# Performance work log

Hardware: AMD Instinct MI355X
Metric: run time of the kernel (lower is better)

The kernel has to match this reference:

```python
import jax, jax.numpy as jnp
import numpy as np

N, E, B = 16000, 256000, 32
IN, HID, H1, OUT, H2 = 768, 256, 4, 128, 2
LN_EPS = 1e-5


def _gat_layer(x, src, dst, W, a_src, a_dst, b, heads, out, n, concat):
    # x: (n, in), W: (heads*out, in), a_src/a_dst: (heads, out), b: (heads*out,) or (out,)
    h = (x @ W.T).reshape(n, heads, out)                      # (n, H, out)
    alpha_s = (h * a_src).sum(-1)                             # (n, H)
    alpha_d = (h * a_dst).sum(-1)                             # (n, H)
    e = jax.nn.leaky_relu(alpha_s[src] + alpha_d[dst], 0.2)   # (E', H)
    # segment softmax over incoming edges of each dst node
    m = jax.ops.segment_max(e, dst, num_segments=n)           # (n, H)
    ex = jnp.exp(e - m[dst])
    den = jax.ops.segment_sum(ex, dst, num_segments=n)
    alpha = ex / (den[dst] + 1e-16)                           # (E', H)
    msg = h[src] * alpha[..., None]                           # (E', H, out)
    agg = jax.ops.segment_sum(msg, dst, num_segments=n)       # (n, H, out)
    o = agg.reshape(n, heads * out) if concat else agg.mean(axis=1)
    return o + b


def setup_inputs() -> dict:
    key = jax.random.key(0)
    ks = jax.random.split(key, 16)
    x = jax.random.normal(ks[0], (N, IN), dtype=jnp.float32)
    edge_index = jax.random.randint(ks[1], (2, E), 0, N, dtype=jnp.int32)
    batch = jnp.sort(jax.random.randint(ks[2], (N,), 0, B, dtype=jnp.int32))
    s = 0.05
    return {
        "x": x, "edge_index": edge_index, "batch": batch,
        "W1": jax.random.normal(ks[3], (H1 * HID, IN), jnp.float32) * s,
        "a1_src": jax.random.normal(ks[4], (H1, HID), jnp.float32) * s,
        "a1_dst": jax.random.normal(ks[5], (H1, HID), jnp.float32) * s,
        "b1": jnp.zeros((H1 * HID,), jnp.float32),
        "W2": jax.random.normal(ks[6], (H2 * OUT, H1 * HID), jnp.float32) * s,
        "a2_src": jax.random.normal(ks[7], (H2, OUT), jnp.float32) * s,
        "a2_dst": jax.random.normal(ks[8], (H2, OUT), jnp.float32) * s,
        "b2": jnp.zeros((OUT,), jnp.float32),
        "proj_W": jax.random.normal(ks[9], (768, OUT), jnp.float32) * s,
        "proj_b": jnp.zeros((768,), jnp.float32),
        "ln_g": jnp.ones((768,), jnp.float32),
        "ln_b": jnp.zeros((768,), jnp.float32),
    }


def reference(x, edge_index, batch, W1, a1_src, a1_dst, b1,
              W2, a2_src, a2_dst, b2, proj_W, proj_b, ln_g, ln_b):
    # add self-loops (PyG GATConv default add_self_loops=True)
    loop = jnp.arange(N, dtype=edge_index.dtype)
    src = jnp.concatenate([edge_index[0], loop])
    dst = jnp.concatenate([edge_index[1], loop])

    h1 = jax.nn.elu(_gat_layer(x, src, dst, W1, a1_src, a1_dst, b1, H1, HID, N, True))
    # dropout = 0 (eval mode)
    h2 = jax.nn.elu(_gat_layer(h1, src, dst, W2, a2_src, a2_dst, b2, H2, OUT, N, False))

    # global mean pool per graph
    sums = jax.ops.segment_sum(h2, batch, num_segments=B)            # (B, OUT)
    cnt = jax.ops.segment_sum(jnp.ones((N,), h2.dtype), batch, num_segments=B)
    pooled = sums / jnp.maximum(cnt, 1.0)[:, None]

    z = pooled @ proj_W.T + proj_b                                   # (B, 768)
    mu = z.mean(-1, keepdims=True)
    var = ((z - mu) ** 2).mean(-1, keepdims=True)
    graph_embed = (z - mu) / jnp.sqrt(var + LN_EPS) * ln_g + ln_b
    return graph_embed, h2
```

## Files before the change

kernel.cpp:

```cpp
#include <hip/hip_runtime.h>
#include <cstddef>

#define NN   16000
#define NE   256000
#define EP   (NE + NN)
#define BG   32
#define IN_F 768
#define HID  256
#define H1C  4
#define F1   (H1C * HID)
#define OUTF 128
#define H2C  2
#define F2   (H2C * OUTF)

typedef __bf16 bf16x8 __attribute__((ext_vector_type(8)));
typedef float  f32x4  __attribute__((ext_vector_type(4)));
typedef unsigned short us8 __attribute__((ext_vector_type(8)));

static __device__ __forceinline__ float lrelu02(float x) { return x > 0.f ? x : 0.2f * x; }
static __device__ __forceinline__ float eluf(float x)    { return x > 0.f ? x : expm1f(x); }
static __device__ __forceinline__ unsigned short rne_bf16(float f) {
    unsigned u = __float_as_uint(f);
    return (unsigned short)((u + 0x7fffu + ((u >> 16) & 1u)) >> 16);
}
static __device__ __forceinline__ float b2f(unsigned short u) {
    return __uint_as_float(((unsigned)u) << 16);
}

#define GLDS16(gp, lp) __builtin_amdgcn_global_load_lds(                         \
    (const __attribute__((address_space(1))) void*)(gp),                          \
    (__attribute__((address_space(3))) void*)(lp), 16, 0, 0)

__global__ __launch_bounds__(256) void k_f2b(const float* __restrict__ in,
                                             unsigned short* __restrict__ out, int n) {
    int i = (blockIdx.x * 256 + threadIdx.x) * 4;
    if (i >= n) return;
    float4 v = *(const float4*)&in[i];
    ushort4 o;
    o.x = rne_bf16(v.x); o.y = rne_bf16(v.y); o.z = rne_bf16(v.z); o.w = rne_bf16(v.w);
    *(ushort4*)&out[i] = o;
}

__global__ void k_hist(const int* __restrict__ ei, int* __restrict__ deg) {
    int e = blockIdx.x * 256 + threadIdx.x;
    if (e >= EP) return;
    int d = (e < NE) ? ei[NE + e] : (e - NE);
    atomicAdd(&deg[d], 1);
}

__global__ void k_scan(const int* __restrict__ deg, int* __restrict__ off, int* __restrict__ cursor) {
    __shared__ int sums[256];
    int t = threadIdx.x;
    const int CH = (NN + 255) / 256;
    int base = t * CH;
    int s = 0;
    for (int i = 0; i < CH; ++i) { int idx = base + i; if (idx < NN) s += deg[idx]; }
    sums[t] = s;
    __syncthreads();
    for (int ofs = 1; ofs < 256; ofs <<= 1) {
        int v = 0;
        if (t >= ofs) v = sums[t - ofs];
        __syncthreads();
        sums[t] += v;
        __syncthreads();
    }
    int run = sums[t] - s;
    for (int i = 0; i < CH; ++i) {
        int idx = base + i;
        if (idx < NN) { off[idx] = run; cursor[idx] = run; run += deg[idx]; }
    }
    if (t == 255) off[NN] = run;
}

__global__ void k_scatter(const int* __restrict__ ei, int* __restrict__ cursor,
                          int* __restrict__ csr_src, int* __restrict__ csr_dst) {
    int e = blockIdx.x * 256 + threadIdx.x;
    if (e >= EP) return;
    int s, d;
    if (e < NE) { s = ei[e]; d = ei[NE + e]; } else { s = d = e - NE; }
    int pos = atomicAdd(&cursor[d], 1);
    csr_src[pos] = s;
    csr_dst[pos] = d;
}

__global__ __launch_bounds__(256) void k_mfma_nt(const unsigned short* __restrict__ A,
                                                 const unsigned short* __restrict__ B,
                                                 unsigned short* __restrict__ C,
                                                 int N, int K) {
    __shared__ __align__(16) unsigned short As[128 * 32];
    __shared__ __align__(16) unsigned short Bs[128 * 32];
    const int t = threadIdx.x;
    const int w = t >> 6, lane = t & 63;
    const int m0 = blockIdx.y * 128, n0 = blockIdx.x * 128;
    const int wm = (w >> 1) * 64, wn = (w & 1) * 64;

    const unsigned short* ga0 = A + (size_t)(m0 + (t >> 2)) * K + (t & 3) * 8;
    const unsigned short* ga1 = ga0 + (size_t)64 * K;
    const unsigned short* gb0 = B + (size_t)(n0 + (t >> 2)) * K + (t & 3) * 8;
    const unsigned short* gb1 = gb0 + (size_t)64 * K;
    unsigned short* lA0 = &As[(w * 64) * 8];
    unsigned short* lA1 = &As[(w * 64 + 256) * 8];
    unsigned short* lB0 = &Bs[(w * 64) * 8];
    unsigned short* lB1 = &Bs[(w * 64 + 256) * 8];

    f32x4 acc[4][4] = {};

    const bf16x8* pa = (const bf16x8*)As + (wm + (lane & 15)) * 4 + (lane >> 4);
    const bf16x8* pb = (const bf16x8*)Bs + (wn + (lane & 15)) * 4 + (lane >> 4);

    for (int k0 = 0; k0 < K; k0 += 32) {
        GLDS16(ga0, lA0); GLDS16(ga1, lA1);
        GLDS16(gb0, lB0); GLDS16(gb1, lB1);
        ga0 += 32; ga1 += 32; gb0 += 32; gb1 += 32;
        __syncthreads();
        bf16x8 a0 = pa[0], a1 = pa[64], a2 = pa[128], a3 = pa[192];
        bf16x8 b0 = pb[0], b1 = pb[64], b2 = pb[128], b3 = pb[192];
        acc[0][0] = __builtin_amdgcn_mfma_f32_16x16x32_bf16(a0, b0, acc[0][0], 0, 0, 0);
        acc[0][1] = __builtin_amdgcn_mfma_f32_16x16x32_bf16(a0, b1, acc[0][1], 0, 0, 0);
        acc[0][2] = __builtin_amdgcn_mfma_f32_16x16x32_bf16(a0, b2, acc[0][2], 0, 0, 0);
        acc[0][3] = __builtin_amdgcn_mfma_f32_16x16x32_bf16(a0, b3, acc[0][3], 0, 0, 0);
        acc[1][0] = __builtin_amdgcn_mfma_f32_16x16x32_bf16(a1, b0, acc[1][0], 0, 0, 0);
        acc[1][1] = __builtin_amdgcn_mfma_f32_16x16x32_bf16(a1, b1, acc[1][1], 0, 0, 0);
        acc[1][2] = __builtin_amdgcn_mfma_f32_16x16x32_bf16(a1, b2, acc[1][2], 0, 0, 0);
        acc[1][3] = __builtin_amdgcn_mfma_f32_16x16x32_bf16(a1, b3, acc[1][3], 0, 0, 0);
        acc[2][0] = __builtin_amdgcn_mfma_f32_16x16x32_bf16(a2, b0, acc[2][0], 0, 0, 0);
        acc[2][1] = __builtin_amdgcn_mfma_f32_16x16x32_bf16(a2, b1, acc[2][1], 0, 0, 0);
        acc[2][2] = __builtin_amdgcn_mfma_f32_16x16x32_bf16(a2, b2, acc[2][2], 0, 0, 0);
        acc[2][3] = __builtin_amdgcn_mfma_f32_16x16x32_bf16(a2, b3, acc[2][3], 0, 0, 0);
        acc[3][0] = __builtin_amdgcn_mfma_f32_16x16x32_bf16(a3, b0, acc[3][0], 0, 0, 0);
        acc[3][1] = __builtin_amdgcn_mfma_f32_16x16x32_bf16(a3, b1, acc[3][1], 0, 0, 0);
        acc[3][2] = __builtin_amdgcn_mfma_f32_16x16x32_bf16(a3, b2, acc[3][2], 0, 0, 0);
        acc[3][3] = __builtin_amdgcn_mfma_f32_16x16x32_bf16(a3, b3, acc[3][3], 0, 0, 0);
        __syncthreads();
    }
    const int ccol = n0 + wn + (lane & 15);
    const int crow = m0 + wm + (lane >> 4) * 4;
#pragma unroll
    for (int mi = 0; mi < 4; ++mi)
#pragma unroll
        for (int i = 0; i < 4; ++i) {
            unsigned short* cp = C + (size_t)(crow + mi * 16 + i) * N + ccol;
            cp[0]  = rne_bf16(acc[mi][0][i]);
            cp[16] = rne_bf16(acc[mi][1][i]);
            cp[32] = rne_bf16(acc[mi][2][i]);
            cp[48] = rne_bf16(acc[mi][3][i]);
        }
}

__global__ __launch_bounds__(256) void k_alpha1(const unsigned short* __restrict__ h,
                                                const float* __restrict__ a_s,
                                                const float* __restrict__ a_d,
                                                float* __restrict__ as_o,
                                                float* __restrict__ ad_o) {
    int n = blockIdx.x;
    int t = threadIdx.x;
    int head = t >> 6;
    int f = t * 4;
    ushort4 hu = *(const ushort4*)&h[(size_t)n * F1 + f];
    float4 sv = *(const float4*)&a_s[f];
    float4 dv = *(const float4*)&a_d[f];
    float hx = b2f(hu.x), hy = b2f(hu.y), hz = b2f(hu.z), hw = b2f(hu.w);
    float ps = hx * sv.x + hy * sv.y + hz * sv.z + hw * sv.w;
    float pd = hx * dv.x + hy * dv.y + hz * dv.z + hw * dv.w;
    for (int ofs = 32; ofs > 0; ofs >>= 1) {
        ps += __shfl_down(ps, ofs);
        pd += __shfl_down(pd, ofs);
    }
    if ((t & 63) == 0) { as_o[n * H1C + head] = ps; ad_o[n * H1C + head] = pd; }
}

__global__ __launch_bounds__(256) void k_alpha2(const unsigned short* __restrict__ h,
                                                const float* __restrict__ a_s,
                                                const float* __restrict__ a_d,
                                                float* __restrict__ as_o,
                                                float* __restrict__ ad_o) {
    int n = blockIdx.x * 4 + (threadIdx.x >> 6);
    int lane = threadIdx.x & 63;
    int f = lane * 4;
    ushort4 hu = *(const ushort4*)&h[(size_t)n * F2 + f];
    float4 sv = *(const float4*)&a_s[f];
    float4 dv = *(const float4*)&a_d[f];
    float hx = b2f(hu.x), hy = b2f(hu.y), hz = b2f(hu.z), hw = b2f(hu.w);
    float ps = hx * sv.x + hy * sv.y + hz * sv.z + hw * sv.w;
    float pd = hx * dv.x + hy * dv.y + hz * dv.z + hw * dv.w;
    for (int ofs = 16; ofs > 0; ofs >>= 1) {
        ps += __shfl_down(ps, ofs, 32);
        pd += __shfl_down(pd, ofs, 32);
    }
    if ((lane & 31) == 0) {
        int head = lane >> 5;
        as_o[n * H2C + head] = ps;
        ad_o[n * H2C + head] = pd;
    }
}

__global__ __launch_bounds__(256) void k_el1(const int* __restrict__ csr_src,
                                             const int* __restrict__ csr_dst,
                                             const float* __restrict__ as1,
                                             const float* __restrict__ ad1,
                                             float* __restrict__ el) {
    int j = blockIdx.x * 256 + threadIdx.x;
    if (j >= EP) return;
    int s = csr_src[j], d = csr_dst[j];
    float4 av = *(const float4*)&as1[s * H1C];
    float4 dv = *(const float4*)&ad1[d * H1C];
    float4 o;
    o.x = lrelu02(av.x + dv.x);
    o.y = lrelu02(av.y + dv.y);
    o.z = lrelu02(av.z + dv.z);
    o.w = lrelu02(av.w + dv.w);
    *(float4*)&el[(size_t)j * 4] = o;
}

__global__ __launch_bounds__(256) void k_el2(const int* __restrict__ csr_src,
                                             const int* __restrict__ csr_dst,
                                             const float* __restrict__ as2,
                                             const float* __restrict__ ad2,
                                             float* __restrict__ el) {
    int j = blockIdx.x * 256 + threadIdx.x;
    if (j >= EP) return;
    int s = csr_src[j], d = csr_dst[j];
    float2 av = *(const float2*)&as2[s * 2];
    float2 dv = *(const float2*)&ad2[d * 2];
    float2 o;
    o.x = lrelu02(av.x + dv.x);
    o.y = lrelu02(av.y + dv.y);
    *(float2*)&el[(size_t)j * 2] = o;
}

__global__ __launch_bounds__(256) void k_gat1(const unsigned short* __restrict__ hb,
                                              const float* __restrict__ el,
                                              const int* __restrict__ off,
                                              const int* __restrict__ csr,
                                              const float* __restrict__ b1,
                                              unsigned short* __restrict__ h1b) {
    const int l = threadIdx.x & 63;
    const int d = blockIdx.x * 4 + (threadIdx.x >> 6);
    const int beg = off[d], end = off[d + 1];
    const int h = l >> 4, sub = l & 15;

    float m0 = -1e30f, m1 = -1e30f, m2 = -1e30f, m3 = -1e30f;
    for (int j = beg + l; j < end; j += 64) {
        float4 e = *(const float4*)&el[(size_t)j * 4];
        m0 = fmaxf(m0, e.x); m1 = fmaxf(m1, e.y);
        m2 = fmaxf(m2, e.z); m3 = fmaxf(m3, e.w);
    }
    for (int o = 32; o > 0; o >>= 1) {
        m0 = fmaxf(m0, __shfl_down(m0, o));
        m1 = fmaxf(m1, __shfl_down(m1, o));
        m2 = fmaxf(m2, __shfl_down(m2, o));
        m3 = fmaxf(m3, __shfl_down(m3, o));
    }
    m0 = __shfl(m0, 0); m1 = __shfl(m1, 0); m2 = __shfl(m2, 0); m3 = __shfl(m3, 0);
    float s0 = 0.f, s1 = 0.f, s2 = 0.f, s3 = 0.f;
    for (int j = beg + l; j < end; j += 64) {
        float4 e = *(const float4*)&el[(size_t)j * 4];
        s0 += expf(e.x - m0); s1 += expf(e.y - m1);
        s2 += expf(e.z - m2); s3 += expf(e.w - m3);
    }
    for (int o = 32; o > 0; o >>= 1) {
        s0 += __shfl_down(s0, o);
        s1 += __shfl_down(s1, o);
        s2 += __shfl_down(s2, o);
        s3 += __shfl_down(s3, o);
    }
    s0 = __shfl(s0, 0); s1 = __shfl(s1, 0); s2 = __shfl(s2, 0); s3 = __shfl(s3, 0);
    float mh  = (h == 0) ? m0 : (h == 1) ? m1 : (h == 2) ? m2 : m3;
    float sh  = (h == 0) ? s0 : (h == 1) ? s1 : (h == 2) ? s2 : s3;
    float rdh = 1.f / (sh + 1e-16f);

    float acc[16] = {};
    const unsigned short* hrow = hb + l * 16;
    for (int cbeg = beg; cbeg < end; cbeg += 16) {
        int cnt = end - cbeg; if (cnt > 16) cnt = 16;
        int idx = cbeg + sub;
        int idxc = idx < end ? idx : end - 1;
        int s_sel = csr[idxc];
        float ev = el[(size_t)idxc * 4 + h];
        float myw = (idx < end) ? expf(ev - mh) * rdh : 0.f;
        for (int jj = 0; jj < cnt; jj += 4) {
            int sa = __shfl(s_sel, jj + 0);
            int sb = __shfl(s_sel, jj + 1);
            int sc = __shfl(s_sel, jj + 2);
            int sd = __shfl(s_sel, jj + 3);
            float wa = __shfl(myw, (h << 4) | (jj + 0));
            float wb = __shfl(myw, (h << 4) | (jj + 1));
            float wc = __shfl(myw, (h << 4) | (jj + 2));
            float wd = __shfl(myw, (h << 4) | (jj + 3));
            const unsigned short* pa_ = hrow + (size_t)sa * F1;
            const unsigned short* pb_ = hrow + (size_t)sb * F1;
            const unsigned short* pc_ = hrow + (size_t)sc * F1;
            const unsigned short* pd_ = hrow + (size_t)sd * F1;
            us8 a0 = *(const us8*)pa_, a1 = *(const us8*)(pa_ + 8);
            us8 b0 = *(const us8*)pb_, b1 = *(const us8*)(pb_ + 8);
            us8 c0 = *(const us8*)pc_, c1 = *(const us8*)(pc_ + 8);
            us8 d0 = *(const us8*)pd_, d1 = *(const us8*)(pd_ + 8);
#pragma unroll
            for (int i = 0; i < 8; ++i) {
                acc[i]     += wa * b2f(a0[i]) + wb * b2f(b0[i]) + wc * b2f(c0[i]) + wd * b2f(d0[i]);
                acc[8 + i] += wa * b2f(a1[i]) + wb * b2f(b1[i]) + wc * b2f(c1[i]) + wd * b2f(d1[i]);
            }
        }
    }
    const int f0 = l * 16;
    us8 o0, o1;
#pragma unroll
    for (int i = 0; i < 8; ++i)  o0[i] = rne_bf16(eluf(acc[i] + b1[f0 + i]));
#pragma unroll
    for (int i = 0; i < 8; ++i)  o1[i] = rne_bf16(eluf(acc[8 + i] + b1[f0 + 8 + i]));
    *(us8*)&h1b[(size_t)d * F1 + f0]     = o0;
    *(us8*)&h1b[(size_t)d * F1 + f0 + 8] = o1;
}

__global__ __launch_bounds__(256) void k_gat2(const unsigned short* __restrict__ h2b,
                                              const float* __restrict__ el,
                                              const int* __restrict__ off,
                                              const int* __restrict__ csr,
                                              const float* __restrict__ b2,
                                              float* __restrict__ out_h2) {
    const int l = threadIdx.x & 63;
    const int d = blockIdx.x * 4 + (threadIdx.x >> 6);
    const int beg = off[d], end = off[d + 1];
    const int c = l & 31, p = l >> 5;
    const int myhead = c >> 4;
    const int hw = p;

    float m0 = -1e30f, m1 = -1e30f;
    for (int j = beg + l; j < end; j += 64) {
        float2 e = *(const float2*)&el[(size_t)j * 2];
        m0 = fmaxf(m0, e.x); m1 = fmaxf(m1, e.y);
    }
    for (int o = 32; o > 0; o >>= 1) {
        m0 = fmaxf(m0, __shfl_down(m0, o));
        m1 = fmaxf(m1, __shfl_down(m1, o));
    }
    m0 = __shfl(m0, 0); m1 = __shfl(m1, 0);
    float s0 = 0.f, s1 = 0.f;
    for (int j = beg + l; j < end; j += 64) {
        float2 e = *(const float2*)&el[(size_t)j * 2];
        s0 += expf(e.x - m0); s1 += expf(e.y - m1);
    }
    for (int o = 32; o > 0; o >>= 1) {
        s0 += __shfl_down(s0, o);
        s1 += __shfl_down(s1, o);
    }
    s0 = __shfl(s0, 0); s1 = __shfl(s1, 0);
    float mhw  = hw ? m1 : m0;
    float shw  = hw ? s1 : s0;
    float rdhw = 1.f / (shw + 1e-16f);

    float acc[8] = {};
    const unsigned short* base = h2b + c * 8;
    for (int cbeg = beg; cbeg < end; cbeg += 32) {
        int cnt = end - cbeg; if (cnt > 32) cnt = 32;
        int idx = cbeg + c;
        int idxc = idx < end ? idx : end - 1;
        int s_sel = csr[idxc];
        float ev = el[(size_t)idxc * 2 + hw];
        float myw = (idx < end) ? expf(ev - mhw) * rdhw : 0.f;
        for (int jj = 0; jj < cnt; jj += 8) {
            int e0 = jj + p * 4;
            int sa = __shfl(s_sel, e0 + 0);
            int sb = __shfl(s_sel, e0 + 1);
            int sc = __shfl(s_sel, e0 + 2);
            int sd = __shfl(s_sel, e0 + 3);
            float wa = __shfl(myw, (myhead << 5) | (e0 + 0));
            float wb = __shfl(myw, (myhead << 5) | (e0 + 1));
            float wc = __shfl(myw, (myhead << 5) | (e0 + 2));
            float wd = __shfl(myw, (myhead << 5) | (e0 + 3));
            us8 va = *(const us8*)(base + (size_t)sa * F2);
            us8 vb = *(const us8*)(base + (size_t)sb * F2);
            us8 vc = *(const us8*)(base + (size_t)sc * F2);
            us8 vd = *(const us8*)(base + (size_t)sd * F2);
#pragma unroll
            for (int i = 0; i < 8; ++i)
                acc[i] += wa * b2f(va[i]) + wb * b2f(vb[i]) + wc * b2f(vc[i]) + wd * b2f(vd[i]);
        }
    }
#pragma unroll
    for (int i = 0; i < 8; ++i) acc[i] += __shfl(acc[i], l ^ 32);
    float pt[8];
#pragma unroll
    for (int i = 0; i < 8; ++i) pt[i] = __shfl(acc[i], l ^ 16);
    if (l < 16) {
        int f = l * 8;
        float o[8];
#pragma unroll
        for (int i = 0; i < 8; ++i) o[i] = eluf(0.5f * (acc[i] + pt[i]) + b2[f + i]);
        *(float4*)&out_h2[(size_t)d * OUTF + f]     = make_float4(o[0], o[1], o[2], o[3]);
        *(float4*)&out_h2[(size_t)d * OUTF + f + 4] = make_float4(o[4], o[5], o[6], o[7]);
    }
}

__global__ __launch_bounds__(256) void k_proj_ln(const float* __restrict__ h2,
                                                 const int* __restrict__ batch,
                                                 const float* __restrict__ pW,
                                                 const float* __restrict__ pb,
                                                 const float* __restrict__ g,
                                                 const float* __restrict__ be,
                                                 float* __restrict__ out) {
    __shared__ float part[256];
    __shared__ float ph[OUTF];
    __shared__ float zb[768];
    __shared__ float red[256];
    __shared__ float s_mu, s_rstd;
    int b = blockIdx.x, t = threadIdx.x;
    int lo = 0, hi = NN;
    while (lo < hi) { int mid = (lo + hi) >> 1; if (batch[mid] < b) lo = mid + 1; else hi = mid; }
    int n0 = lo;
    lo = 0; hi = NN;
    while (lo < hi) { int mid = (lo + hi) >> 1; if (batch[mid] < b + 1) lo = mid + 1; else hi = mid; }
    int n1 = lo;
    {
        int f = t & 127, half = t >> 7;
        float a0 = 0.f, a1 = 0.f, a2 = 0.f, a3 = 0.f;
        int n = n0 + half;
        for (; n + 6 < n1; n += 8) {
            a0 += h2[(size_t)n * OUTF + f];
            a1 += h2[(size_t)(n + 2) * OUTF + f];
            a2 += h2[(size_t)(n + 4) * OUTF + f];
            a3 += h2[(size_t)(n + 6) * OUTF + f];
        }
        for (; n < n1; n += 2) a0 += h2[(size_t)n * OUTF + f];
        part[t] = a0 + a1 + a2 + a3;
    }
    __syncthreads();
    if (t < OUTF) {
        float c = (float)(n1 - n0);
        c = c < 1.f ? 1.f : c;
        ph[t] = (part[t] + part[t + 128]) / c;
    }
    __syncthreads();
    for (int r = 0; r < 3; ++r) {
        int j = t + 256 * r;
        float acc = pb[j];
        for (int k = 0; k < OUTF; k += 4) {
            float4 w = *(const float4*)&pW[(size_t)j * OUTF + k];
            acc += w.x * ph[k] + w.y * ph[k + 1] + w.z * ph[k + 2] + w.w * ph[k + 3];
        }
        zb[j] = acc;
    }
    __syncthreads();
    float s = zb[t] + zb[t + 256] + zb[t + 512];
    red[t] = s;
    __syncthreads();
    for (int ofs = 128; ofs > 0; ofs >>= 1) {
        if (t < ofs) red[t] += red[t + ofs];
        __syncthreads();
    }
    if (t == 0) s_mu = red[0] / 768.f;
    __syncthreads();
    float mu = s_mu;
    float d0 = zb[t] - mu, d1 = zb[t + 256] - mu, d2 = zb[t + 512] - mu;
    red[t] = d0 * d0 + d1 * d1 + d2 * d2;
    __syncthreads();
    for (int ofs = 128; ofs > 0; ofs >>= 1) {
        if (t < ofs) red[t] += red[t + ofs];
        __syncthreads();
    }
    if (t == 0) s_rstd = rsqrtf(red[0] / 768.f + 1e-5f);
    __syncthreads();
    float rstd = s_rstd;
    for (int r = 0; r < 3; ++r) {
        int j = t + 256 * r;
        out[(size_t)b * 768 + j] = (zb[j] - mu) * rstd * g[j] + be[j];
    }
}

extern "C" void kernel_launch(void* const* d_in, const int* in_sizes, int n_in,
                              void* d_out, int out_size, void* d_ws, size_t ws_size,
                              hipStream_t stream) {
    const float* x    = (const float*)d_in[0];
    const int*   ei   = (const int*)d_in[1];
    const int*   batch= (const int*)d_in[2];
    const float* W1   = (const float*)d_in[3];
    const float* a1s  = (const float*)d_in[4];
    const float* a1d  = (const float*)d_in[5];
    const float* b1   = (const float*)d_in[6];
    const float* W2   = (const float*)d_in[7];
    const float* a2s  = (const float*)d_in[8];
    const float* a2d  = (const float*)d_in[9];
    const float* b2   = (const float*)d_in[10];
    const float* pW   = (const float*)d_in[11];
    const float* pb   = (const float*)d_in[12];
    const float* lng  = (const float*)d_in[13];
    const float* lnb  = (const float*)d_in[14];

    float* out_ge = (float*)d_out;
    float* out_h2 = (float*)d_out + BG * 768;

    char* w = (char*)d_ws;
    unsigned short* xb   = (unsigned short*)w;  w += (size_t)NN * IN_F * 2;
    unsigned short* W1b  = (unsigned short*)w;  w += (size_t)F1 * IN_F * 2;
    unsigned short* W2b  = (unsigned short*)w;  w += (size_t)F2 * F1 * 2;
    unsigned short* hbufb= (unsigned short*)w;  w += (size_t)NN * F1 * 2;
    unsigned short* h1b  = (unsigned short*)w;  w += (size_t)NN * F1 * 2;
    unsigned short* h2b  = (unsigned short*)w;  w += (size_t)NN * F2 * 2;
    float* as1  = (float*)w;  w += (size_t)NN * H1C * 4;
    float* ad1  = (float*)w;  w += (size_t)NN * H1C * 4;
    float* as2  = (float*)w;  w += (size_t)NN * H2C * 4;
    float* ad2  = (float*)w;  w += (size_t)NN * H2C * 4;
    int* deg    = (int*)w;    w += (size_t)NN * 4;
    int* off    = (int*)w;    w += (size_t)(NN + 4) * 4;
    int* cursor = (int*)w;    w += (size_t)NN * 4;
    int* csr    = (int*)w;    w += (size_t)EP * 4;
    int* csrd   = (int*)w;    w += (size_t)EP * 4;
    float* el1  = (float*)w;  w += (size_t)EP * H1C * 4;
    float* el2  = (float*)w;  w += (size_t)EP * H2C * 4;

    hipMemsetAsync(deg, 0, NN * 4, stream);

    k_f2b<<<(NN * IN_F) / 1024, 256, 0, stream>>>(x, xb, NN * IN_F);
    k_f2b<<<(F1 * IN_F) / 1024, 256, 0, stream>>>(W1, W1b, F1 * IN_F);
    k_f2b<<<(F2 * F1) / 1024, 256, 0, stream>>>(W2, W2b, F2 * F1);

    k_hist<<<(EP + 255) / 256, 256, 0, stream>>>(ei, deg);
    k_scan<<<1, 256, 0, stream>>>(deg, off, cursor);
    k_scatter<<<(EP + 255) / 256, 256, 0, stream>>>(ei, cursor, csr, csrd);

    k_mfma_nt<<<dim3(F1 / 128, NN / 128), 256, 0, stream>>>(xb, W1b, hbufb, F1, IN_F);
    k_alpha1<<<NN, 256, 0, stream>>>(hbufb, a1s, a1d, as1, ad1);
    k_el1<<<(EP + 255) / 256, 256, 0, stream>>>(csr, csrd, as1, ad1, el1);
    k_gat1<<<NN / 4, 256, 0, stream>>>(hbufb, el1, off, csr, b1, h1b);

    k_mfma_nt<<<dim3(F2 / 128, NN / 128), 256, 0, stream>>>(h1b, W2b, h2b, F2, F1);
    k_alpha2<<<NN / 4, 256, 0, stream>>>(h2b, a2s, a2d, as2, ad2);
    k_el2<<<(EP + 255) / 256, 256, 0, stream>>>(csr, csrd, as2, ad2, el2);
    k_gat2<<<NN / 4, 256, 0, stream>>>(h2b, el2, off, csr, b2, out_h2);

    k_proj_ln<<<BG, 256, 0, stream>>>(out_h2, batch, pW, pb, lng, lnb, out_ge);
}
```

Baseline: 454.5 us.

## Widen parallelism in GAT1 aggregation, scan and pooling/LayerNorm kernels

GAT layer-1 aggregation now uses two waves per destination node, each covering two heads and 8 features per lane, which doubles the number of waves in flight for the gather. The single-block degree scan goes from 256 to 1024 threads, shortening each thread's serial chunk. The pool/projection/LayerNorm kernel goes from 256 to 1024 threads per graph to spread the node-sum and projection work. The cost is redundant softmax max/sum passes, since each half-node wave recomputes its heads' statistics and the edge list is walked twice per node.

```diff
diff --git a/kernel.cpp b/kernel.cpp
--- a/kernel.cpp
+++ b/kernel.cpp
@@ -48,16 +48,17 @@
     atomicAdd(&deg[d], 1);
 }
 
-__global__ void k_scan(const int* __restrict__ deg, int* __restrict__ off, int* __restrict__ cursor) {
-    __shared__ int sums[256];
+__global__ __launch_bounds__(1024) void k_scan(const int* __restrict__ deg,
+                                               int* __restrict__ off, int* __restrict__ cursor) {
+    __shared__ int sums[1024];
     int t = threadIdx.x;
-    const int CH = (NN + 255) / 256;
+    const int CH = 16;
     int base = t * CH;
     int s = 0;
     for (int i = 0; i < CH; ++i) { int idx = base + i; if (idx < NN) s += deg[idx]; }
     sums[t] = s;
     __syncthreads();
-    for (int ofs = 1; ofs < 256; ofs <<= 1) {
+    for (int ofs = 1; ofs < 1024; ofs <<= 1) {
         int v = 0;
         if (t >= ofs) v = sums[t - ofs];
         __syncthreads();
@@ -69,7 +70,7 @@
         int idx = base + i;
         if (idx < NN) { off[idx] = run; cursor[idx] = run; run += deg[idx]; }
     }
-    if (t == 255) off[NN] = run;
+    if (t == 1023) off[NN] = run;
 }
 
 __global__ void k_scatter(const int* __restrict__ ei, int* __restrict__ cursor,
@@ -235,45 +236,41 @@
                                               const float* __restrict__ b1,
                                               unsigned short* __restrict__ h1b) {
     const int l = threadIdx.x & 63;
-    const int d = blockIdx.x * 4 + (threadIdx.x >> 6);
+    const int w = threadIdx.x >> 6;
+    const int d = blockIdx.x * 2 + (w >> 1);
+    const int hf = w & 1;
     const int beg = off[d], end = off[d + 1];
-    const int h = l >> 4, sub = l & 15;
-
-    float m0 = -1e30f, m1 = -1e30f, m2 = -1e30f, m3 = -1e30f;
+    const int h = hf * 2 + (l >> 5);
+    const int f0 = hf * 512 + l * 8;
+
+    float mA = -1e30f, mB = -1e30f;
     for (int j = beg + l; j < end; j += 64) {
-        float4 e = *(const float4*)&el[(size_t)j * 4];
-        m0 = fmaxf(m0, e.x); m1 = fmaxf(m1, e.y);
-        m2 = fmaxf(m2, e.z); m3 = fmaxf(m3, e.w);
+        float2 e = *(const float2*)&el[(size_t)j * 4 + hf * 2];
+        mA = fmaxf(mA, e.x); mB = fmaxf(mB, e.y);
     }
     for (int o = 32; o > 0; o >>= 1) {
-        m0 = fmaxf(m0, __shfl_down(m0, o));
-        m1 = fmaxf(m1, __shfl_down(m1, o));
-        m2 = fmaxf(m2, __shfl_down(m2, o));
-        m3 = fmaxf(m3, __shfl_down(m3, o));
-    }
-    m0 = __shfl(m0, 0); m1 = __shfl(m1, 0); m2 = __shfl(m2, 0); m3 = __shfl(m3, 0);
-    float s0 = 0.f, s1 = 0.f, s2 = 0.f, s3 = 0.f;
+        mA = fmaxf(mA, __shfl_down(mA, o));
+        mB = fmaxf(mB, __shfl_down(mB, o));
+    }
+    mA = __shfl(mA, 0); mB = __shfl(mB, 0);
+    float sA = 0.f, sB = 0.f;
     for (int j = beg + l; j < end; j += 64) {
-        float4 e = *(const float4*)&el[(size_t)j * 4];
-        s0 += expf(e.x - m0); s1 += expf(e.y - m1);
-        s2 += expf(e.z - m2); s3 += expf(e.w - m3);
+        float2 e = *(const float2*)&el[(size_t)j * 4 + hf * 2];
+        sA += expf(e.x - mA); sB += expf(e.y - mB);
     }
     for (int o = 32; o > 0; o >>= 1) {
-        s0 += __shfl_down(s0, o);
-        s1 += __shfl_down(s1, o);
-        s2 += __shfl_down(s2, o);
-        s3 += __shfl_down(s3, o);
-    }
-    s0 = __shfl(s0, 0); s1 = __shfl(s1, 0); s2 = __shfl(s2, 0); s3 = __shfl(s3, 0);
-    float mh  = (h == 0) ? m0 : (h == 1) ? m1 : (h == 2) ? m2 : m3;
-    float sh  = (h == 0) ? s0 : (h == 1) ? s1 : (h == 2) ? s2 : s3;
-    float rdh = 1.f / (sh + 1e-16f);
-
-    float acc[16] = {};
-    const unsigned short* hrow = hb + l * 16;
-    for (int cbeg = beg; cbeg < end; cbeg += 16) {
-        int cnt = end - cbeg; if (cnt > 16) cnt = 16;
-        int idx = cbeg + sub;
+        sA += __shfl_down(sA, o);
+        sB += __shfl_down(sB, o);
+    }
+    sA = __shfl(sA, 0); sB = __shfl(sB, 0);
+    float mh  = (l < 32) ? mA : mB;
+    float rdh = 1.f / (((l < 32) ? sA : sB) + 1e-16f);
+
+    float acc[8] = {};
+    const unsigned short* hrow = hb + f0;
+    for (int cbeg = beg; cbeg < end; cbeg += 32) {
+        int cnt = end - cbeg; if (cnt > 32) cnt = 32;
+        int idx = cbeg + (l & 31);
         int idxc = idx < end ? idx : end - 1;
         int s_sel = csr[idxc];
         float ev = el[(size_t)idxc * 4 + h];
@@ -283,33 +280,23 @@
             int sb = __shfl(s_sel, jj + 1);
             int sc = __shfl(s_sel, jj + 2);
             int sd = __shfl(s_sel, jj + 3);
-            float wa = __shfl(myw, (h << 4) | (jj + 0));
-            float wb = __shfl(myw, (h << 4) | (jj + 1));
-            float wc = __shfl(myw, (h << 4) | (jj + 2));
-            float wd = __shfl(myw, (h << 4) | (jj + 3));
-            const unsigned short* pa_ = hrow + (size_t)sa * F1;
-            const unsigned short* pb_ = hrow + (size_t)sb * F1;
-            const unsigned short* pc_ = hrow + (size_t)sc * F1;
-            const unsigned short* pd_ = hrow + (size_t)sd * F1;
-            us8 a0 = *(const us8*)pa_, a1 = *(const us8*)(pa_ + 8);
-            us8 b0 = *(const us8*)pb_, b1 = *(const us8*)(pb_ + 8);
-            us8 c0 = *(const us8*)pc_, c1 = *(const us8*)(pc_ + 8);
-            us8 d0 = *(const us8*)pd_, d1 = *(const us8*)(pd_ + 8);
-#pragma unroll
-            for (int i = 0; i < 8; ++i) {
-                acc[i]     += wa * b2f(a0[i]) + wb * b2f(b0[i]) + wc * b2f(c0[i]) + wd * b2f(d0[i]);
-                acc[8 + i] += wa * b2f(a1[i]) + wb * b2f(b1[i]) + wc * b2f(c1[i]) + wd * b2f(d1[i]);
-            }
+            float wa = __shfl(myw, (l & 32) | (jj + 0));
+            float wb = __shfl(myw, (l & 32) | (jj + 1));
+            float wc = __shfl(myw, (l & 32) | (jj + 2));
+            float wd = __shfl(myw, (l & 32) | (jj + 3));
+            us8 va = *(const us8*)(hrow + (size_t)sa * F1);
+            us8 vb = *(const us8*)(hrow + (size_t)sb * F1);
+            us8 vc = *(const us8*)(hrow + (size_t)sc * F1);
+            us8 vd = *(const us8*)(hrow + (size_t)sd * F1);
+#pragma unroll
+            for (int i = 0; i < 8; ++i)
+                acc[i] += wa * b2f(va[i]) + wb * b2f(vb[i]) + wc * b2f(vc[i]) + wd * b2f(vd[i]);
         }
     }
-    const int f0 = l * 16;
-    us8 o0, o1;
-#pragma unroll
-    for (int i = 0; i < 8; ++i)  o0[i] = rne_bf16(eluf(acc[i] + b1[f0 + i]));
-#pragma unroll
-    for (int i = 0; i < 8; ++i)  o1[i] = rne_bf16(eluf(acc[8 + i] + b1[f0 + 8 + i]));
-    *(us8*)&h1b[(size_t)d * F1 + f0]     = o0;
-    *(us8*)&h1b[(size_t)d * F1 + f0 + 8] = o1;
+    us8 ob;
+#pragma unroll
+    for (int i = 0; i < 8; ++i) ob[i] = rne_bf16(eluf(acc[i] + b1[f0 + i]));
+    *(us8*)&h1b[(size_t)d * F1 + f0] = ob;
 }
 
 __global__ __launch_bounds__(256) void k_gat2(const unsigned short* __restrict__ h2b,
@@ -392,17 +379,17 @@
     }
 }
 
-__global__ __launch_bounds__(256) void k_proj_ln(const float* __restrict__ h2,
-                                                 const int* __restrict__ batch,
-                                                 const float* __restrict__ pW,
-                                                 const float* __restrict__ pb,
-                                                 const float* __restrict__ g,
-                                                 const float* __restrict__ be,
-                                                 float* __restrict__ out) {
-    __shared__ float part[256];
+__global__ __launch_bounds__(1024) void k_proj_ln(const float* __restrict__ h2,
+                                                  const int* __restrict__ batch,
+                                                  const float* __restrict__ pW,
+                                                  const float* __restrict__ pb,
+                                                  const float* __restrict__ g,
+                                                  const float* __restrict__ be,
+                                                  float* __restrict__ out) {
+    __shared__ float part[1024];
     __shared__ float ph[OUTF];
     __shared__ float zb[768];
-    __shared__ float red[256];
+    __shared__ float red[1024];
     __shared__ float s_mu, s_rstd;
     int b = blockIdx.x, t = threadIdx.x;
     int lo = 0, hi = NN;
@@ -412,59 +399,51 @@
     while (lo < hi) { int mid = (lo + hi) >> 1; if (batch[mid] < b + 1) lo = mid + 1; else hi = mid; }
     int n1 = lo;
     {
-        int f = t & 127, half = t >> 7;
-        float a0 = 0.f, a1 = 0.f, a2 = 0.f, a3 = 0.f;
-        int n = n0 + half;
-        for (; n + 6 < n1; n += 8) {
-            a0 += h2[(size_t)n * OUTF + f];
-            a1 += h2[(size_t)(n + 2) * OUTF + f];
-            a2 += h2[(size_t)(n + 4) * OUTF + f];
-            a3 += h2[(size_t)(n + 6) * OUTF + f];
-        }
-        for (; n < n1; n += 2) a0 += h2[(size_t)n * OUTF + f];
-        part[t] = a0 + a1 + a2 + a3;
+        int f = t & 127, slot = t >> 7;
+        float a = 0.f;
+        for (int n = n0 + slot; n < n1; n += 8) a += h2[(size_t)n * OUTF + f];
+        part[t] = a;
     }
     __syncthreads();
     if (t < OUTF) {
+        float s = 0.f;
+#pragma unroll
+        for (int k = 0; k < 8; ++k) s += part[k * 128 + t];
         float c = (float)(n1 - n0);
         c = c < 1.f ? 1.f : c;
-        ph[t] = (part[t] + part[t + 128]) / c;
-    }
-    __syncthreads();
-    for (int r = 0; r < 3; ++r) {
-        int j = t + 256 * r;
-        float acc = pb[j];
+        ph[t] = s / c;
+    }
+    __syncthreads();
+    if (t < 768) {
+        float acc = pb[t];
         for (int k = 0; k < OUTF; k += 4) {
-            float4 w = *(const float4*)&pW[(size_t)j * OUTF + k];
+            float4 w = *(const float4*)&pW[(size_t)t * OUTF + k];
             acc += w.x * ph[k] + w.y * ph[k + 1] + w.z * ph[k + 2] + w.w * ph[k + 3];
         }
-        zb[j] = acc;
-    }
-    __syncthreads();
-    float s = zb[t] + zb[t + 256] + zb[t + 512];
-    red[t] = s;
-    __syncthreads();
-    for (int ofs = 128; ofs > 0; ofs >>= 1) {
+        zb[t] = acc;
+    }
+    __syncthreads();
+    red[t] = (t < 768) ? zb[t] : 0.f;
+    __syncthreads();
+    for (int ofs = 512; ofs > 0; ofs >>= 1) {
         if (t < ofs) red[t] += red[t + ofs];
         __syncthreads();
     }
     if (t == 0) s_mu = red[0] / 768.f;
     __syncthreads();
     float mu = s_mu;
-    float d0 = zb[t] - mu, d1 = zb[t + 256] - mu, d2 = zb[t + 512] - mu;
-    red[t] = d0 * d0 + d1 * d1 + d2 * d2;
-    __syncthreads();
-    for (int ofs = 128; ofs > 0; ofs >>= 1) {
+    float dv = (t < 768) ? (zb[t] - mu) : 0.f;
+    red[t] = dv * dv;
+    __syncthreads();
+    for (int ofs = 512; ofs > 0; ofs >>= 1) {
         if (t < ofs) red[t] += red[t + ofs];
         __syncthreads();
     }
     if (t == 0) s_rstd = rsqrtf(red[0] / 768.f + 1e-5f);
     __syncthreads();
     float rstd = s_rstd;
-    for (int r = 0; r < 3; ++r) {
-        int j = t + 256 * r;
-        out[(size_t)b * 768 + j] = (zb[j] - mu) * rstd * g[j] + be[j];
-    }
+    if (t < 768)
+        out[(size_t)b * 768 + t] = (zb[t] - mu) * rstd * g[t] + be[t];
 }
 
 extern "C" void kernel_launch(void* const* d_in, const int* in_sizes, int n_in,
@@ -515,18 +494,18 @@
     k_f2b<<<(F2 * F1) / 1024, 256, 0, stream>>>(W2, W2b, F2 * F1);
 
     k_hist<<<(EP + 255) / 256, 256, 0, stream>>>(ei, deg);
-    k_scan<<<1, 256, 0, stream>>>(deg, off, cursor);
+    k_scan<<<1, 1024, 0, stream>>>(deg, off, cursor);
     k_scatter<<<(EP + 255) / 256, 256, 0, stream>>>(ei, cursor, csr, csrd);
 
     k_mfma_nt<<<dim3(F1 / 128, NN / 128), 256, 0, stream>>>(xb, W1b, hbufb, F1, IN_F);
     k_alpha1<<<NN, 256, 0, stream>>>(hbufb, a1s, a1d, as1, ad1);
     k_el1<<<(EP + 255) / 256, 256, 0, stream>>>(csr, csrd, as1, ad1, el1);
-    k_gat1<<<NN / 4, 256, 0, stream>>>(hbufb, el1, off, csr, b1, h1b);
+    k_gat1<<<NN / 2, 256, 0, stream>>>(hbufb, el1, off, csr, b1, h1b);
 
     k_mfma_nt<<<dim3(F2 / 128, NN / 128), 256, 0, stream>>>(h1b, W2b, h2b, F2, F1);
     k_alpha2<<<NN / 4, 256, 0, stream>>>(h2b, a2s, a2d, as2, ad2);
     k_el2<<<(EP + 255) / 256, 256, 0, stream>>>(csr, csrd, as2, ad2, el2);
     k_gat2<<<NN / 4, 256, 0, stream>>>(h2b, el2, off, csr, b2, out_h2);
 
-    k_proj_ln<<<BG, 256, 0, stream>>>(out_h2, batch, pW, pb, lng, lnb, out_ge);
-}
+    k_proj_ln<<<BG, 1024, 0, stream>>>(out_h2, batch, pW, pb, lng, lnb, out_ge);
+}
```

After: 429.5 us. -5.5%, faster.
